# Optimization experiments

Measured on AMD Instinct MI355X. Metric: run time of the kernel, lower is better.

## Reference

```python
import jax, jax.numpy as jnp
import numpy as np

EPS = 1e-5
N_HEADS = 4
N_GROUPS = 32


def group_norm(x, gamma, beta, num_groups):
    # x: (B, C, H, W)
    B, C, H, W = x.shape
    xg = x.reshape(B, num_groups, (C // num_groups) * H * W)
    mean = xg.mean(axis=2, keepdims=True)
    var = xg.var(axis=2, keepdims=True)
    xn = ((xg - mean) * jax.lax.rsqrt(var + EPS)).reshape(B, C, H, W)
    return xn * gamma[None, :, None, None] + beta[None, :, None, None]


def conv1x1(x, W, b=None):
    # 1x1 conv == channel-mixing matmul: (O,C) x (B,C,H,W) -> (B,O,H,W)
    y = jnp.einsum('oc,bchw->bohw', W, x)
    if b is not None:
        y = y + b[None, :, None, None]
    return y


def setup_inputs() -> dict:
    key = jax.random.key(0)
    ks = jax.random.split(key, 8)
    B, Cq, Cc, H, W = 2, 128, 128, 64, 64
    x = jax.random.normal(ks[0], (B, Cq, H, W), dtype=jnp.float32)
    context = jax.random.normal(ks[1], (B, Cc, H, W), dtype=jnp.float32)
    sq = Cq ** -0.5
    sc = Cc ** -0.5
    return {
        'x': x,
        'context': context,
        'gq': jnp.ones((Cq,), jnp.float32),
        'bq': jnp.zeros((Cq,), jnp.float32),
        'gctx': jnp.ones((Cc,), jnp.float32),
        'bctx': jnp.zeros((Cc,), jnp.float32),
        'Wq': jax.random.normal(ks[2], (Cq, Cq), jnp.float32) * sq,
        'Wk': jax.random.normal(ks[3], (Cq, Cc), jnp.float32) * sc,
        'Wv': jax.random.normal(ks[4], (Cq, Cc), jnp.float32) * sc,
        'Wout': jax.random.normal(ks[5], (Cq, Cq), jnp.float32) * 0.02,
        'bout': jnp.zeros((Cq,), jnp.float32),
        'alpha': jnp.asarray(1.0, jnp.float32),
    }


def reference(x, context, gq, bq, gctx, bctx, Wq, Wk, Wv, Wout, bout, alpha):
    B, C, H, W = x.shape
    hd = C // N_HEADS
    # QKV projections (GroupNorm + 1x1 conv); note v uses raw context (no norm)
    q = conv1x1(group_norm(x, gq, bq, N_GROUPS), Wq)
    k = conv1x1(group_norm(context, gctx, bctx, N_GROUPS), Wk)
    v = conv1x1(context, Wv)
    q = q.reshape(B, N_HEADS, hd, H * W)
    k = k.reshape(B, N_HEADS, hd, H * W)
    v = v.reshape(B, N_HEADS, hd, H * W)
    scale = jnp.asarray(hd ** 0.5, x.dtype)
    attn = jnp.einsum('bncd,bnce->bnde', q, k) / scale  # (B, nH, HW, HW)
    attn = jax.nn.softmax(attn, axis=-1)
    out = jnp.einsum('bnde,bnce->bncd', attn, v).reshape(B, C, H, W)
    return x + alpha * conv1x1(out, Wout, bout)
```

## Files before the change

### kernel.cpp

```cpp
#include <hip/hip_runtime.h>
#include <hip/hip_bf16.h>
#include <math.h>

#define L 4096
#define C 128
#define NH 4
#define HD 32
#define KS 2
#define EPSV 1e-5f

typedef short bf16x8 __attribute__((ext_vector_type(8)));
typedef float f32x4 __attribute__((ext_vector_type(4)));

static __device__ __forceinline__ unsigned pack2bf(float a, float b) {
    __hip_bfloat162 h = __float22bfloat162_rn(make_float2(a, b));
    unsigned u; __builtin_memcpy(&u, &h, 4); return u;
}

__global__ __launch_bounds__(256) void gn_stats_kernel(
    const float* __restrict__ x, const float* __restrict__ ctx,
    float* __restrict__ stats)
{
    int bid = blockIdx.x;
    int t = threadIdx.x;
    const float* in = (bid < 64) ? x : ctx;
    int rem = bid & 63;
    const float4* p = (const float4*)(in + (size_t)rem * 16384);
    float s = 0.f, s2 = 0.f;
    for (int i = t; i < 4096; i += 256) {
        float4 v = p[i];
        s  += v.x + v.y + v.z + v.w;
        s2 += v.x*v.x + v.y*v.y + v.z*v.z + v.w*v.w;
    }
    #pragma unroll
    for (int m = 32; m >= 1; m >>= 1) {
        s  += __shfl_xor(s, m);
        s2 += __shfl_xor(s2, m);
    }
    __shared__ float wsum[4][2];
    int w = t >> 6;
    if ((t & 63) == 0) { wsum[w][0] = s; wsum[w][1] = s2; }
    __syncthreads();
    if (t == 0) {
        float S = wsum[0][0] + wsum[1][0] + wsum[2][0] + wsum[3][0];
        float S2 = wsum[0][1] + wsum[1][1] + wsum[2][1] + wsum[3][1];
        float mean = S * (1.f / 16384.f);
        float var = S2 * (1.f / 16384.f) - mean * mean;
        stats[bid * 2]     = mean;
        stats[bid * 2 + 1] = rsqrtf(var + EPSV);
    }
}

__global__ __launch_bounds__(256) void proj_kernel(
    const float* __restrict__ x, const float* __restrict__ ctx,
    const float* __restrict__ gq, const float* __restrict__ bq,
    const float* __restrict__ gctx, const float* __restrict__ bctx,
    const float* __restrict__ stats,
    const float* __restrict__ Wq, const float* __restrict__ Wk,
    const float* __restrict__ Wv,
    unsigned short* __restrict__ Qt, unsigned short* __restrict__ Kt,
    unsigned short* __restrict__ Vsw)
{
    int t = threadIdx.x;
    int w = t >> 6, lane = t & 63, n16 = lane & 15, quad = lane >> 4;
    int dtile = blockIdx.x * 32;
    int b = blockIdx.y, z = blockIdx.z;

    const float* in; const float* Wm; const float* gamma; const float* beta;
    int sel = 1, donorm = 1; float oscale = 1.f;
    if (z == 0)      { in = x;   Wm = Wq; gamma = gq;   beta = bq;   sel = 0;
                       oscale = 0.17677669529663689f * 1.4426950408889634f; }
    else if (z == 1) { in = ctx; Wm = Wk; gamma = gctx; beta = bctx; }
    else             { in = ctx; Wm = Wv; gamma = 0;    beta = 0;    donorm = 0; }

    __shared__ __attribute__((aligned(16))) unsigned short Xs[32 * 136];

    {
        int c0 = (t >> 3) * 4, d4 = (t & 7) * 4;
        const float* inb = in + (size_t)b * (C * L);
        float vv[4][4];
        #pragma unroll
        for (int j = 0; j < 4; j++) {
            int c = c0 + j;
            float sc = 1.f, sh = 0.f;
            if (donorm) {
                int sidx = (sel * 64 + b * 32 + (c >> 2)) * 2;
                float mean = stats[sidx], inv = stats[sidx + 1];
                sc = inv * gamma[c];
                sh = beta[c] - mean * sc;
            }
            float4 v = *(const float4*)(inb + (size_t)c * L + dtile + d4);
            vv[j][0] = v.x * sc + sh; vv[j][1] = v.y * sc + sh;
            vv[j][2] = v.z * sc + sh; vv[j][3] = v.w * sc + sh;
        }
        #pragma unroll
        for (int i = 0; i < 4; i++) {
            uint2 pk;
            pk.x = pack2bf(vv[0][i], vv[1][i]);
            pk.y = pack2bf(vv[2][i], vv[3][i]);
            *(uint2*)&Xs[(d4 + i) * 136 + c0] = pk;
        }
    }

    bf16x8 wa[2][4];
    #pragma unroll
    for (int os2 = 0; os2 < 2; os2++) {
        const float* wr = Wm + (size_t)(((w + os2 * 4) * 16) + n16) * C + quad * 8;
        #pragma unroll
        for (int kk = 0; kk < 4; kk++) {
            float4 a  = *(const float4*)(wr + kk * 32);
            float4 b2 = *(const float4*)(wr + kk * 32 + 4);
            unsigned u4[4] = { pack2bf(a.x, a.y),  pack2bf(a.z, a.w),
                               pack2bf(b2.x, b2.y), pack2bf(b2.z, b2.w) };
            __builtin_memcpy(&wa[os2][kk], u4, 16);
        }
    }
    __syncthreads();

    f32x4 zero = {0.f, 0.f, 0.f, 0.f};
    f32x4 acc[2][2];
    acc[0][0] = zero; acc[0][1] = zero; acc[1][0] = zero; acc[1][1] = zero;
    #pragma unroll
    for (int kk = 0; kk < 4; kk++) {
        #pragma unroll
        for (int dg = 0; dg < 2; dg++) {
            bf16x8 xb;
            uint4 u = *(const uint4*)&Xs[(dg * 16 + n16) * 136 + kk * 32 + quad * 8];
            __builtin_memcpy(&xb, &u, 16);
            acc[0][dg] = __builtin_amdgcn_mfma_f32_16x16x32_bf16(wa[0][kk], xb, acc[0][dg], 0, 0, 0);
            acc[1][dg] = __builtin_amdgcn_mfma_f32_16x16x32_bf16(wa[1][kk], xb, acc[1][dg], 0, 0, 0);
        }
    }

    #pragma unroll
    for (int os2 = 0; os2 < 2; os2++) {
        int o = ((w + os2 * 4) * 16) + quad * 4;
        int h = o >> 5, c32 = o & 31;
        #pragma unroll
        for (int dg = 0; dg < 2; dg++) {
            int d = dtile + dg * 16 + n16;
            if (z < 2) {
                unsigned short* outp = (z == 0) ? Qt : Kt;
                uint2 pk;
                pk.x = pack2bf(acc[os2][dg][0] * oscale, acc[os2][dg][1] * oscale);
                pk.y = pack2bf(acc[os2][dg][2] * oscale, acc[os2][dg][3] * oscale);
                *(uint2*)(outp + ((size_t)(b * NH + h) * L + d) * HD + c32) = pk;
            } else {
                unsigned short* vb = Vsw + (size_t)(b * NH + h) * (L * HD)
                                   + (size_t)(d >> 3) * 256 + (d & 7);
                #pragma unroll
                for (int r = 0; r < 4; r++) {
                    __hip_bfloat16 hv = __float2bfloat16(acc[os2][dg][r]);
                    unsigned short us; __builtin_memcpy(&us, &hv, 2);
                    vb[(c32 + r) * 8] = us;
                }
            }
        }
    }
}

__global__ __launch_bounds__(256, 4) void flash_kernel(
    const unsigned short* __restrict__ Qt, const unsigned short* __restrict__ Kt,
    const unsigned short* __restrict__ Vsw, float* __restrict__ Po,
    float* __restrict__ Pl)
{
    __shared__ __attribute__((aligned(16))) unsigned short Ps[4 * 16 * 72];

    int t = threadIdx.x;
    int w = t >> 6, lane = t & 63;
    int n16 = lane & 15, quad = lane >> 4;
    int bh = blockIdx.x;
    int qstrip = blockIdx.y * 4 + w;
    int ks = blockIdx.z;
    size_t hb = (size_t)bh * (L * HD);

    bf16x8 qf;
    {
        uint4 u = *(const uint4*)(Qt + hb + (size_t)(qstrip * 16 + n16) * HD + quad * 8);
        __builtin_memcpy(&qf, &u, 16);
    }

    const unsigned short* kfp = Kt + hb + (size_t)n16 * HD + quad * 8;
    const unsigned short* vfp = Vsw + hb + quad * 256 + n16 * 8;

    int e0 = ks * (L / KS);

    bf16x8 ka[2][4], va[2][4];
    #pragma unroll
    for (int et = 0; et < 4; et++) {
        uint4 u = *(const uint4*)(kfp + (size_t)(e0 + et * 16) * HD);
        __builtin_memcpy(&ka[0][et], &u, 16);
    }
    #pragma unroll
    for (int es = 0; es < 2; es++)
        #pragma unroll
        for (int f = 0; f < 2; f++) {
            uint4 u = *(const uint4*)(vfp + (size_t)(e0 + es * 32) * 32 + f * 128);
            __builtin_memcpy(&va[0][es * 2 + f], &u, 16);
        }

    float lsum = 0.f;
    f32x4 zero = {0.f, 0.f, 0.f, 0.f};
    f32x4 oacc0 = zero, oacc1 = zero;
    unsigned short* pw = &Ps[w * 1152 + n16 * 72];

    #pragma unroll 2
    for (int kt = 0; kt < L / KS / 64; kt++) {
        int cur = kt & 1, nxt = cur ^ 1;
        int e1 = e0 + (kt + 1) * 64;
        #pragma unroll
        for (int et = 0; et < 4; et++) {
            uint4 u = *(const uint4*)(kfp + (size_t)(e1 + et * 16) * HD);
            __builtin_memcpy(&ka[nxt][et], &u, 16);
        }
        #pragma unroll
        for (int es = 0; es < 2; es++)
            #pragma unroll
            for (int f = 0; f < 2; f++) {
                uint4 u = *(const uint4*)(vfp + (size_t)(e1 + es * 32) * 32 + f * 128);
                __builtin_memcpy(&va[nxt][es * 2 + f], &u, 16);
            }

        f32x4 s[4];
        #pragma unroll
        for (int et = 0; et < 4; et++)
            s[et] = __builtin_amdgcn_mfma_f32_16x16x32_bf16(ka[cur][et], qf, zero, 0, 0, 0);

        float p[4][4];
        #pragma unroll
        for (int et = 0; et < 4; et++)
            #pragma unroll
            for (int r = 0; r < 4; r++) {
                p[et][r] = __builtin_amdgcn_exp2f(s[et][r]);
                lsum += p[et][r];
            }

        #pragma unroll
        for (int et = 0; et < 4; et++) {
            uint2 pk;
            pk.x = pack2bf(p[et][0], p[et][1]);
            pk.y = pack2bf(p[et][2], p[et][3]);
            *(uint2*)(pw + et * 16 + quad * 4) = pk;
        }

        #pragma unroll
        for (int es = 0; es < 2; es++) {
            bf16x8 pf;
            uint4 u = *(const uint4*)(pw + es * 32 + quad * 8);
            __builtin_memcpy(&pf, &u, 16);
            oacc0 = __builtin_amdgcn_mfma_f32_16x16x32_bf16(va[cur][es * 2 + 0], pf, oacc0, 0, 0, 0);
            oacc1 = __builtin_amdgcn_mfma_f32_16x16x32_bf16(va[cur][es * 2 + 1], pf, oacc1, 0, 0, 0);
        }
    }

    lsum += __shfl_xor(lsum, 16);
    lsum += __shfl_xor(lsum, 32);

    int dq = qstrip * 16 + n16;
    float* po = Po + (((size_t)(bh * KS + ks) * L + dq) * 32);
    *(float4*)(po + quad * 4)      = make_float4(oacc0[0], oacc0[1], oacc0[2], oacc0[3]);
    *(float4*)(po + 16 + quad * 4) = make_float4(oacc1[0], oacc1[1], oacc1[2], oacc1[3]);
    if (quad == 0)
        Pl[(size_t)(bh * KS + ks) * L + dq] = lsum;
}

__global__ __launch_bounds__(256) void final_kernel(
    const float* __restrict__ Po, const float* __restrict__ Pl,
    const float* __restrict__ x, const float* __restrict__ Wout,
    const float* __restrict__ bout, const float* __restrict__ alpha,
    float* __restrict__ out)
{
    int t = threadIdx.x;
    int w = t >> 6, lane = t & 63, n16 = lane & 15, quad = lane >> 4;
    int dtile = blockIdx.x * 32;
    int b = blockIdx.y;

    __shared__ __attribute__((aligned(16))) float Ot[128 * 36];
    unsigned short* Xs = (unsigned short*)Ot;

    {
        int c0 = (t >> 3) * 4, d4 = (t & 7) * 4;
        int bh = b * NH + (c0 >> 5);
        int c32 = c0 & 31;
        #pragma unroll
        for (int i = 0; i < 4; i++) {
            int dq = dtile + d4 + i;
            float l0 = Pl[(size_t)(bh * KS + 0) * L + dq];
            float l1 = Pl[(size_t)(bh * KS + 1) * L + dq];
            float rl = 1.f / (l0 + l1);
            float4 p0 = *(const float4*)(Po + ((size_t)(bh * KS + 0) * L + dq) * 32 + c32);
            float4 p1 = *(const float4*)(Po + ((size_t)(bh * KS + 1) * L + dq) * 32 + c32);
            uint2 pk;
            pk.x = pack2bf((p0.x + p1.x) * rl, (p0.y + p1.y) * rl);
            pk.y = pack2bf((p0.z + p1.z) * rl, (p0.w + p1.w) * rl);
            *(uint2*)&Xs[(d4 + i) * 136 + c0] = pk;
        }
    }

    bf16x8 wa[2][4];
    #pragma unroll
    for (int os2 = 0; os2 < 2; os2++) {
        const float* wr = Wout + (size_t)(((w + os2 * 4) * 16) + n16) * C + quad * 8;
        #pragma unroll
        for (int kk = 0; kk < 4; kk++) {
            float4 a  = *(const float4*)(wr + kk * 32);
            float4 b2 = *(const float4*)(wr + kk * 32 + 4);
            unsigned u4[4] = { pack2bf(a.x, a.y),  pack2bf(a.z, a.w),
                               pack2bf(b2.x, b2.y), pack2bf(b2.z, b2.w) };
            __builtin_memcpy(&wa[os2][kk], u4, 16);
        }
    }
    __syncthreads();

    f32x4 zero = {0.f, 0.f, 0.f, 0.f};
    f32x4 acc[2][2];
    acc[0][0] = zero; acc[0][1] = zero; acc[1][0] = zero; acc[1][1] = zero;
    #pragma unroll
    for (int kk = 0; kk < 4; kk++) {
        #pragma unroll
        for (int dg = 0; dg < 2; dg++) {
            bf16x8 xb;
            uint4 u = *(const uint4*)&Xs[(dg * 16 + n16) * 136 + kk * 32 + quad * 8];
            __builtin_memcpy(&xb, &u, 16);
            acc[0][dg] = __builtin_amdgcn_mfma_f32_16x16x32_bf16(wa[0][kk], xb, acc[0][dg], 0, 0, 0);
            acc[1][dg] = __builtin_amdgcn_mfma_f32_16x16x32_bf16(wa[1][kk], xb, acc[1][dg], 0, 0, 0);
        }
    }
    __syncthreads();

    #pragma unroll
    for (int os2 = 0; os2 < 2; os2++) {
        int o = ((w + os2 * 4) * 16) + quad * 4;
        #pragma unroll
        for (int dg = 0; dg < 2; dg++) {
            int dl = dg * 16 + n16;
            #pragma unroll
            for (int r = 0; r < 4; r++)
                Ot[(o + r) * 36 + dl] = acc[os2][dg][r];
        }
    }
    __syncthreads();

    float al = alpha[0];
    int o = t >> 1, dl0 = (t & 1) * 16;
    float bo = bout[o];
    const float* xb = x + ((size_t)b * C + o) * L + dtile + dl0;
    float* ob = out + ((size_t)b * C + o) * L + dtile + dl0;
    #pragma unroll
    for (int jj = 0; jj < 4; jj++) {
        float4 a  = *(const float4*)&Ot[o * 36 + dl0 + jj * 4];
        float4 xv = *(const float4*)(xb + jj * 4);
        float4 r;
        r.x = xv.x + al * (a.x + bo);
        r.y = xv.y + al * (a.y + bo);
        r.z = xv.z + al * (a.z + bo);
        r.w = xv.w + al * (a.w + bo);
        *(float4*)(ob + jj * 4) = r;
    }
}

extern "C" void kernel_launch(void* const* d_in, const int* in_sizes, int n_in,
                              void* d_out, int out_size, void* d_ws, size_t ws_size,
                              hipStream_t stream) {
    const float* x     = (const float*)d_in[0];
    const float* ctx   = (const float*)d_in[1];
    const float* gq    = (const float*)d_in[2];
    const float* bq    = (const float*)d_in[3];
    const float* gctx  = (const float*)d_in[4];
    const float* bctx  = (const float*)d_in[5];
    const float* Wq    = (const float*)d_in[6];
    const float* Wk    = (const float*)d_in[7];
    const float* Wv    = (const float*)d_in[8];
    const float* Wout  = (const float*)d_in[9];
    const float* bout  = (const float*)d_in[10];
    const float* alpha = (const float*)d_in[11];
    float* out = (float*)d_out;

    char* ws = (char*)d_ws;
    unsigned short* Qt  = (unsigned short*)(ws);
    unsigned short* Kt  = (unsigned short*)(ws + 2097152);
    unsigned short* Vsw = (unsigned short*)(ws + 4194304);
    float*          Po  = (float*)(ws + 6291456);
    float*          Pl  = (float*)(ws + 14680064);
    float*          stats = (float*)(ws + 14942208);

    gn_stats_kernel<<<128, 256, 0, stream>>>(x, ctx, stats);
    proj_kernel<<<dim3(128, 2, 3), 256, 0, stream>>>(x, ctx, gq, bq, gctx, bctx,
                                                     stats, Wq, Wk, Wv, Qt, Kt, Vsw);
    flash_kernel<<<dim3(8, 64, KS), 256, 0, stream>>>(Qt, Kt, Vsw, Po, Pl);
    final_kernel<<<dim3(128, 2), 256, 0, stream>>>(Po, Pl, x, Wout, bout, alpha, out);
}
```

Before: 148.2 us.

## Double flash key splits, store partial outputs in bf16, shrink final tiles

Raises the flash-attention key split count from 2 to 4, which doubles the grid and raises the occupancy hint to 8 blocks per CU for better latency hiding. The partial outputs are stored as bf16 instead of fp32 so the larger split does not grow the traffic to the combine step. The final kernel now sums a variable number of splits, reads 8 channels per thread, and uses 16-column tiles so twice as many blocks run. The cost is extra partial-sum reads and reduced precision in the partial accumulators. The higher occupancy target may also force register spills in the flash kernel.

```diff
diff --git a/kernel.cpp b/kernel.cpp
--- a/kernel.cpp
+++ b/kernel.cpp
@@ -6,7 +6,7 @@
 #define C 128
 #define NH 4
 #define HD 32
-#define KS 2
+#define KS 4
 #define EPSV 1e-5f
 
 typedef short bf16x8 __attribute__((ext_vector_type(8)));
@@ -15,6 +15,12 @@
 static __device__ __forceinline__ unsigned pack2bf(float a, float b) {
     __hip_bfloat162 h = __float22bfloat162_rn(make_float2(a, b));
     unsigned u; __builtin_memcpy(&u, &h, 4); return u;
+}
+static __device__ __forceinline__ float bf_lo(unsigned u) {
+    unsigned v = u << 16; float f; __builtin_memcpy(&f, &v, 4); return f;
+}
+static __device__ __forceinline__ float bf_hi(unsigned u) {
+    unsigned v = u & 0xffff0000u; float f; __builtin_memcpy(&f, &v, 4); return f;
 }
 
 __global__ __launch_bounds__(256) void gn_stats_kernel(
@@ -159,9 +165,9 @@
     }
 }
 
-__global__ __launch_bounds__(256, 4) void flash_kernel(
+__global__ __launch_bounds__(256, 8) void flash_kernel(
     const unsigned short* __restrict__ Qt, const unsigned short* __restrict__ Kt,
-    const unsigned short* __restrict__ Vsw, float* __restrict__ Po,
+    const unsigned short* __restrict__ Vsw, unsigned short* __restrict__ Po,
     float* __restrict__ Pl)
 {
     __shared__ __attribute__((aligned(16))) unsigned short Ps[4 * 16 * 72];
@@ -257,44 +263,54 @@
     lsum += __shfl_xor(lsum, 32);
 
     int dq = qstrip * 16 + n16;
-    float* po = Po + (((size_t)(bh * KS + ks) * L + dq) * 32);
-    *(float4*)(po + quad * 4)      = make_float4(oacc0[0], oacc0[1], oacc0[2], oacc0[3]);
-    *(float4*)(po + 16 + quad * 4) = make_float4(oacc1[0], oacc1[1], oacc1[2], oacc1[3]);
+    unsigned short* po = Po + ((size_t)(bh * KS + ks) * L + dq) * 32;
+    uint2 pk0, pk1;
+    pk0.x = pack2bf(oacc0[0], oacc0[1]); pk0.y = pack2bf(oacc0[2], oacc0[3]);
+    pk1.x = pack2bf(oacc1[0], oacc1[1]); pk1.y = pack2bf(oacc1[2], oacc1[3]);
+    *(uint2*)(po + quad * 4)      = pk0;
+    *(uint2*)(po + 16 + quad * 4) = pk1;
     if (quad == 0)
         Pl[(size_t)(bh * KS + ks) * L + dq] = lsum;
 }
 
 __global__ __launch_bounds__(256) void final_kernel(
-    const float* __restrict__ Po, const float* __restrict__ Pl,
+    const unsigned short* __restrict__ Po, const float* __restrict__ Pl,
     const float* __restrict__ x, const float* __restrict__ Wout,
     const float* __restrict__ bout, const float* __restrict__ alpha,
     float* __restrict__ out)
 {
     int t = threadIdx.x;
     int w = t >> 6, lane = t & 63, n16 = lane & 15, quad = lane >> 4;
-    int dtile = blockIdx.x * 32;
+    int dtile = blockIdx.x * 16;
     int b = blockIdx.y;
 
-    __shared__ __attribute__((aligned(16))) float Ot[128 * 36];
+    __shared__ __attribute__((aligned(16))) float Ot[128 * 20];
     unsigned short* Xs = (unsigned short*)Ot;
 
     {
-        int c0 = (t >> 3) * 4, d4 = (t & 7) * 4;
+        int d_l = t >> 4, c0 = (t & 15) * 8;
+        int dq = dtile + d_l;
         int bh = b * NH + (c0 >> 5);
         int c32 = c0 & 31;
-        #pragma unroll
-        for (int i = 0; i < 4; i++) {
-            int dq = dtile + d4 + i;
-            float l0 = Pl[(size_t)(bh * KS + 0) * L + dq];
-            float l1 = Pl[(size_t)(bh * KS + 1) * L + dq];
-            float rl = 1.f / (l0 + l1);
-            float4 p0 = *(const float4*)(Po + ((size_t)(bh * KS + 0) * L + dq) * 32 + c32);
-            float4 p1 = *(const float4*)(Po + ((size_t)(bh * KS + 1) * L + dq) * 32 + c32);
-            uint2 pk;
-            pk.x = pack2bf((p0.x + p1.x) * rl, (p0.y + p1.y) * rl);
-            pk.y = pack2bf((p0.z + p1.z) * rl, (p0.w + p1.w) * rl);
-            *(uint2*)&Xs[(d4 + i) * 136 + c0] = pk;
-        }
+        float l = 0.f;
+        float o8[8] = {0.f, 0.f, 0.f, 0.f, 0.f, 0.f, 0.f, 0.f};
+        #pragma unroll
+        for (int ks = 0; ks < KS; ks++) {
+            size_t base = (size_t)(bh * KS + ks) * L + dq;
+            l += Pl[base];
+            uint4 u = *(const uint4*)(Po + base * 32 + c32);
+            o8[0] += bf_lo(u.x); o8[1] += bf_hi(u.x);
+            o8[2] += bf_lo(u.y); o8[3] += bf_hi(u.y);
+            o8[4] += bf_lo(u.z); o8[5] += bf_hi(u.z);
+            o8[6] += bf_lo(u.w); o8[7] += bf_hi(u.w);
+        }
+        float rl = 1.f / l;
+        uint4 pk;
+        pk.x = pack2bf(o8[0] * rl, o8[1] * rl);
+        pk.y = pack2bf(o8[2] * rl, o8[3] * rl);
+        pk.z = pack2bf(o8[4] * rl, o8[5] * rl);
+        pk.w = pack2bf(o8[6] * rl, o8[7] * rl);
+        *(uint4*)&Xs[d_l * 136 + c0] = pk;
     }
 
     bf16x8 wa[2][4];
@@ -313,18 +329,15 @@
     __syncthreads();
 
     f32x4 zero = {0.f, 0.f, 0.f, 0.f};
-    f32x4 acc[2][2];
-    acc[0][0] = zero; acc[0][1] = zero; acc[1][0] = zero; acc[1][1] = zero;
+    f32x4 acc[2];
+    acc[0] = zero; acc[1] = zero;
     #pragma unroll
     for (int kk = 0; kk < 4; kk++) {
-        #pragma unroll
-        for (int dg = 0; dg < 2; dg++) {
-            bf16x8 xb;
-            uint4 u = *(const uint4*)&Xs[(dg * 16 + n16) * 136 + kk * 32 + quad * 8];
-            __builtin_memcpy(&xb, &u, 16);
-            acc[0][dg] = __builtin_amdgcn_mfma_f32_16x16x32_bf16(wa[0][kk], xb, acc[0][dg], 0, 0, 0);
-            acc[1][dg] = __builtin_amdgcn_mfma_f32_16x16x32_bf16(wa[1][kk], xb, acc[1][dg], 0, 0, 0);
-        }
+        bf16x8 xb;
+        uint4 u = *(const uint4*)&Xs[n16 * 136 + kk * 32 + quad * 8];
+        __builtin_memcpy(&xb, &u, 16);
+        acc[0] = __builtin_amdgcn_mfma_f32_16x16x32_bf16(wa[0][kk], xb, acc[0], 0, 0, 0);
+        acc[1] = __builtin_amdgcn_mfma_f32_16x16x32_bf16(wa[1][kk], xb, acc[1], 0, 0, 0);
     }
     __syncthreads();
 
@@ -332,24 +345,20 @@
     for (int os2 = 0; os2 < 2; os2++) {
         int o = ((w + os2 * 4) * 16) + quad * 4;
         #pragma unroll
-        for (int dg = 0; dg < 2; dg++) {
-            int dl = dg * 16 + n16;
-            #pragma unroll
-            for (int r = 0; r < 4; r++)
-                Ot[(o + r) * 36 + dl] = acc[os2][dg][r];
-        }
+        for (int r = 0; r < 4; r++)
+            Ot[(o + r) * 20 + n16] = acc[os2][r];
     }
     __syncthreads();
 
     float al = alpha[0];
-    int o = t >> 1, dl0 = (t & 1) * 16;
+    int o = t >> 1, dh = (t & 1) * 8;
     float bo = bout[o];
-    const float* xb = x + ((size_t)b * C + o) * L + dtile + dl0;
-    float* ob = out + ((size_t)b * C + o) * L + dtile + dl0;
-    #pragma unroll
-    for (int jj = 0; jj < 4; jj++) {
-        float4 a  = *(const float4*)&Ot[o * 36 + dl0 + jj * 4];
-        float4 xv = *(const float4*)(xb + jj * 4);
+    const float* xb2 = x + ((size_t)b * C + o) * L + dtile + dh;
+    float* ob = out + ((size_t)b * C + o) * L + dtile + dh;
+    #pragma unroll
+    for (int jj = 0; jj < 2; jj++) {
+        float4 a  = *(const float4*)&Ot[o * 20 + dh + jj * 4];
+        float4 xv = *(const float4*)(xb2 + jj * 4);
         float4 r;
         r.x = xv.x + al * (a.x + bo);
         r.y = xv.y + al * (a.y + bo);
@@ -380,13 +389,13 @@
     unsigned short* Qt  = (unsigned short*)(ws);
     unsigned short* Kt  = (unsigned short*)(ws + 2097152);
     unsigned short* Vsw = (unsigned short*)(ws + 4194304);
-    float*          Po  = (float*)(ws + 6291456);
+    unsigned short* Po  = (unsigned short*)(ws + 6291456);
     float*          Pl  = (float*)(ws + 14680064);
-    float*          stats = (float*)(ws + 14942208);
+    float*          stats = (float*)(ws + 15204352);
 
     gn_stats_kernel<<<128, 256, 0, stream>>>(x, ctx, stats);
     proj_kernel<<<dim3(128, 2, 3), 256, 0, stream>>>(x, ctx, gq, bq, gctx, bctx,
                                                      stats, Wq, Wk, Wv, Qt, Kt, Vsw);
     flash_kernel<<<dim3(8, 64, KS), 256, 0, stream>>>(Qt, Kt, Vsw, Po, Pl);
-    final_kernel<<<dim3(128, 2), 256, 0, stream>>>(Po, Pl, x, Wout, bout, alpha, out);
-}
+    final_kernel<<<dim3(256, 2), 256, 0, stream>>>(Po, Pl, x, Wout, bout, alpha, out);
+}
```

After: 161.5 us. 9.0% more time.
